# Kernel optimization log

Hardware: AMD Instinct MI355X
Metric: run time of the kernel (lower is better)

Reference implementation:

```python
import jax, jax.numpy as jnp
import numpy as np

N, E, IN, H, OUT, L = 50000, 640000, 64, 128, 128, 4
EPS = 1e-8


def setup_inputs() -> dict:
    key = jax.random.key(0)
    ks = jax.random.split(key, 14)
    rn = lambda k, shp: (jax.random.normal(k, shp, jnp.float32) * 0.05)
    return {
        "h": jax.random.normal(ks[0], (N, IN), jnp.float32),
        "pos": jax.random.normal(ks[1], (N, 3), jnp.float32),
        "edge_index": jax.random.randint(ks[2], (2, E), 0, N),
        "emb_W": rn(ks[3], (IN, H)), "emb_b": jnp.zeros((H,), jnp.float32),
        "msg_W1": rn(ks[4], (L, 2 * H + 1, H)), "msg_b1": jnp.zeros((L, H), jnp.float32),
        "msg_W2": rn(ks[5], (L, H, H)), "msg_b2": jnp.zeros((L, H), jnp.float32),
        "coord_W1": rn(ks[6], (L, H, H)), "coord_b1": jnp.zeros((L, H), jnp.float32),
        "coord_W2": rn(ks[7], (L, H, 1)), "coord_b2": jnp.zeros((L, 1), jnp.float32),
        "node_W1": rn(ks[8], (L, 2 * H, H)), "node_b1": jnp.zeros((L, H), jnp.float32),
        "node_W2": rn(ks[9], (L, H, H)), "node_b2": jnp.zeros((L, H), jnp.float32),
        "out_W1": rn(ks[10], (H, H)), "out_b1": jnp.zeros((H,), jnp.float32),
        "out_W2": rn(ks[11], (H, OUT)), "out_b2": jnp.zeros((OUT,), jnp.float32),
    }


def _egnn_forward(h, pos, src, dst, emb_W, emb_b, msg_W1, msg_b1, msg_W2, msg_b2,
                  coord_W1, coord_b1, coord_W2, coord_b2, node_W1, node_b1,
                  node_W2, node_b2, out_W1, out_b1, out_W2, out_b2):
    n = h.shape[0]
    h = h @ emb_W + emb_b  # node embedding [N, H]
    for l in range(L):
        hi, hj = h[dst], h[src]                     # target i, source j gathers [Etot, H]
        rel = pos[src] - pos[dst]                   # row - col (used for coord update)
        dist = jnp.linalg.norm(rel, axis=-1, keepdims=True)  # symmetric, same as |pos_i - pos_j|
        # message MLP: Linear -> SiLU -> Linear -> SiLU on [h_i, h_j, dist]
        m = jax.nn.silu(jnp.concatenate([hi, hj, dist], axis=-1) @ msg_W1[l] + msg_b1[l])
        m = jax.nn.silu(m @ msg_W2[l] + msg_b2[l])
        agg = jax.ops.segment_sum(m, dst, num_segments=n)  # scatter-add to targets
        # coord update: weights from h[row]=h_j, scatter to col=dst
        w = jax.nn.silu(hj @ coord_W1[l] + coord_b1[l]) @ coord_W2[l] + coord_b2[l]  # [Etot,1]
        coord_diff = w * rel / (dist + EPS)
        pos = pos + jax.ops.segment_sum(coord_diff, dst, num_segments=n)
        # node update with residual
        nh = jax.nn.silu(jnp.concatenate([h, agg], axis=-1) @ node_W1[l] + node_b1[l]) @ node_W2[l] + node_b2[l]
        h = h + nh
    out = jax.nn.silu(h @ out_W1 + out_b1) @ out_W2 + out_b2
    return out, pos


def reference(h, pos, edge_index, emb_W, emb_b, msg_W1, msg_b1, msg_W2, msg_b2,
              coord_W1, coord_b1, coord_W2, coord_b2, node_W1, node_b1,
              node_W2, node_b2, out_W1, out_b1, out_W2, out_b2):
    n = h.shape[0]
    loops = jnp.arange(n)  # add_self_loops
    src = jnp.concatenate([edge_index[0], loops])
    dst = jnp.concatenate([edge_index[1], loops])
    return _egnn_forward(h, pos, src, dst, emb_W, emb_b, msg_W1, msg_b1, msg_W2,
                         msg_b2, coord_W1, coord_b1, coord_W2, coord_b2, node_W1,
                         node_b1, node_W2, node_b2, out_W1, out_b1, out_W2, out_b2)
```

## Files before the change

### kernel.cpp

```cpp
#include <hip/hip_runtime.h>
#include <hip/hip_bf16.h>

#define EPSV 1e-8f

typedef short bf16x8 __attribute__((ext_vector_type(8)));
typedef float f32x4  __attribute__((ext_vector_type(4)));

__device__ __forceinline__ float silu_f(float x) {
    return x * __builtin_amdgcn_rcpf(1.0f + __expf(-x));
}
__device__ __forceinline__ float bf2f(short v) {
    return __uint_as_float(((unsigned int)(unsigned short)v) << 16);
}
__device__ __forceinline__ short f2bfs(float f) {
    __hip_bfloat16 h = __float2bfloat16(f);
    return *(short*)&h;
}

#define MAXM 24
struct PackArgs {
    const float* src[MAXM];
    unsigned int doff[MAXM];
    int nchunk[MAXM];
    int nmat;
};

__global__ __launch_bounds__(256) void repack_kernel(PackArgs pa, __hip_bfloat16* base)
{
    int bid = blockIdx.x;
    int m = 0, c = bid;
    while (m < pa.nmat && c >= pa.nchunk[m]) { c -= pa.nchunk[m]; ++m; }
    const float* src = pa.src[m];
    __hip_bfloat16* dst = base + pa.doff[m] + (size_t)c * 4096;
    for (int o = threadIdx.x; o < 4096; o += 256) {
        int j = o & 7, n = (o >> 3) & 127, g = o >> 10;
        dst[o] = __float2bfloat16(src[(size_t)(c * 32 + g * 8 + j) * 128 + n]);
    }
}

__global__ __launch_bounds__(256) void hist_kernel(
    const int* __restrict__ ei, int* __restrict__ cnt, int E, int N)
{
    int e = blockIdx.x * 256 + threadIdx.x;
    int Etot = E + N;
    if (e < Etot) {
        int d = (e < E) ? ei[E + e] : (e - E);
        atomicAdd(&cnt[d], 1);
    }
}

__global__ __launch_bounds__(256) void scan_block_kernel(
    const int* __restrict__ cnt, int* __restrict__ off, int* __restrict__ part, int n)
{
    __shared__ int sdata[256];
    const int tid = threadIdx.x;
    const int base = blockIdx.x * 4096 + tid * 16;
    int loc[16]; int s = 0;
    #pragma unroll
    for (int i = 0; i < 16; ++i) {
        int idx = base + i;
        int v = (idx < n) ? cnt[idx] : 0;
        loc[i] = s; s += v;
    }
    sdata[tid] = s;
    __syncthreads();
    for (int st = 1; st < 256; st <<= 1) {
        int v = (tid >= st) ? sdata[tid - st] : 0;
        __syncthreads();
        sdata[tid] += v;
        __syncthreads();
    }
    int texc = (tid > 0) ? sdata[tid - 1] : 0;
    #pragma unroll
    for (int i = 0; i < 16; ++i) {
        int idx = base + i;
        if (idx < n) off[idx] = texc + loc[i];
    }
    if (tid == 255) part[blockIdx.x] = sdata[255];
}

__global__ void scan_part_kernel(int* part, int np)
{
    if (threadIdx.x == 0 && blockIdx.x == 0) {
        int run = 0;
        for (int i = 0; i < np; ++i) { int v = part[i]; part[i] = run; run += v; }
    }
}

__global__ __launch_bounds__(256) void scan_add_kernel(
    int* __restrict__ off, const int* __restrict__ part, int n)
{
    int idx = blockIdx.x * 4096 + threadIdx.x * 16;
    int p = part[blockIdx.x];
    #pragma unroll
    for (int i = 0; i < 16; ++i)
        if (idx + i < n) off[idx + i] += p;
}

__global__ __launch_bounds__(256) void scatter_kernel(
    const int* __restrict__ ei, int* __restrict__ off,
    int* __restrict__ esrc, int* __restrict__ edst, int E, int N)
{
    int e = blockIdx.x * 256 + threadIdx.x;
    int Etot = E + N;
    if (e < Etot) {
        int s, d;
        if (e < E) { s = ei[e]; d = ei[E + e]; }
        else       { s = d = e - E; }
        int p = atomicAdd(&off[d], 1);
        esrc[p] = s; edst[p] = d;
    }
}

template<int LDA>
__device__ __forceinline__ void mfma_gemm(const __hip_bfloat16 (*At)[LDA], int acol0,
                                          const __hip_bfloat16* __restrict__ Bp,
                                          int kchunks, int w, int lane, f32x4 acc[4][2])
{
    const int ar = lane & 15, g = lane >> 4;
    const int bc = w * 32 + (lane & 15);
    for (int c = 0; c < kchunks; ++c) {
        const int ao = acol0 + c * 32 + g * 8;
        bf16x8 a0 = *(const bf16x8*)&At[ar +  0][ao];
        bf16x8 a1 = *(const bf16x8*)&At[ar + 16][ao];
        bf16x8 a2 = *(const bf16x8*)&At[ar + 32][ao];
        bf16x8 a3 = *(const bf16x8*)&At[ar + 48][ao];
        const __hip_bfloat16* bb = Bp + ((size_t)((c * 4 + g) * 128) + bc) * 8;
        bf16x8 b0 = *(const bf16x8*)(bb);
        bf16x8 b1 = *(const bf16x8*)(bb + 128);
        acc[0][0] = __builtin_amdgcn_mfma_f32_16x16x32_bf16(a0, b0, acc[0][0], 0, 0, 0);
        acc[1][0] = __builtin_amdgcn_mfma_f32_16x16x32_bf16(a1, b0, acc[1][0], 0, 0, 0);
        acc[2][0] = __builtin_amdgcn_mfma_f32_16x16x32_bf16(a2, b0, acc[2][0], 0, 0, 0);
        acc[3][0] = __builtin_amdgcn_mfma_f32_16x16x32_bf16(a3, b0, acc[3][0], 0, 0, 0);
        acc[0][1] = __builtin_amdgcn_mfma_f32_16x16x32_bf16(a0, b1, acc[0][1], 0, 0, 0);
        acc[1][1] = __builtin_amdgcn_mfma_f32_16x16x32_bf16(a1, b1, acc[1][1], 0, 0, 0);
        acc[2][1] = __builtin_amdgcn_mfma_f32_16x16x32_bf16(a2, b1, acc[2][1], 0, 0, 0);
        acc[3][1] = __builtin_amdgcn_mfma_f32_16x16x32_bf16(a3, b1, acc[3][1], 0, 0, 0);
    }
}

__device__ __forceinline__ void zacc(f32x4 acc[4][2]) {
    #pragma unroll
    for (int r = 0; r < 4; ++r)
        #pragma unroll
        for (int c = 0; c < 2; ++c) acc[r][c] = (f32x4){0.f, 0.f, 0.f, 0.f};
}

__device__ __forceinline__ void gemm4x4(const float* __restrict__ Wg,
                                        const float* a0p, const float* a1p,
                                        const float* a2p, const float* a3p,
                                        int K, int o0, float acc[4][4]) {
    for (int k = 0; k < K; k += 4) {
        float4 a0 = *(const float4*)(a0p + k);
        float4 a1 = *(const float4*)(a1p + k);
        float4 a2 = *(const float4*)(a2p + k);
        float4 a3 = *(const float4*)(a3p + k);
        float4 w0 = *(const float4*)(Wg + (k + 0) * 128 + o0);
        float4 w1 = *(const float4*)(Wg + (k + 1) * 128 + o0);
        float4 w2 = *(const float4*)(Wg + (k + 2) * 128 + o0);
        float4 w3 = *(const float4*)(Wg + (k + 3) * 128 + o0);
        float av[4][4] = {{a0.x, a0.y, a0.z, a0.w}, {a1.x, a1.y, a1.z, a1.w},
                          {a2.x, a2.y, a2.z, a2.w}, {a3.x, a3.y, a3.z, a3.w}};
        float wv[4][4] = {{w0.x, w0.y, w0.z, w0.w}, {w1.x, w1.y, w1.z, w1.w},
                          {w2.x, w2.y, w2.z, w2.w}, {w3.x, w3.y, w3.z, w3.w}};
        #pragma unroll
        for (int i = 0; i < 4; ++i)
            #pragma unroll
            for (int kk = 0; kk < 4; ++kk)
                #pragma unroll
                for (int j = 0; j < 4; ++j)
                    acc[i][j] = fmaf(av[i][kk], wv[kk][j], acc[i][j]);
    }
}

__global__ __launch_bounds__(256) void embed_kernel(
    const float* __restrict__ hin, const float* __restrict__ W,
    const float* __restrict__ b, float* __restrict__ hbuf,
    __hip_bfloat16* __restrict__ h16, int N)
{
    __shared__ float in_tile[32][68];
    const int t = threadIdx.x;
    const int nb = blockIdx.x * 32;

    #pragma unroll
    for (int it = 0; it < 2; ++it) {
        int flat = t + 256 * it;
        int c = flat & 15, e = flat >> 4;
        int node = nb + e; if (node >= N) node = N - 1;
        *(float4*)(&in_tile[e][c * 4]) = *(const float4*)(hin + (size_t)node * 64 + c * 4);
    }
    __syncthreads();

    const int o0 = (t & 31) * 4;
    const int e0 = (t >> 5) * 4;
    float acc[4][4];
    #pragma unroll
    for (int i = 0; i < 4; ++i)
        #pragma unroll
        for (int j = 0; j < 4; ++j) acc[i][j] = 0.f;
    gemm4x4(W, &in_tile[e0][0], &in_tile[e0 + 1][0], &in_tile[e0 + 2][0], &in_tile[e0 + 3][0],
            64, o0, acc);
    float4 bv = *(const float4*)(b + o0);
    #pragma unroll
    for (int i = 0; i < 4; ++i) {
        int node = nb + e0 + i;
        if (node < N) {
            float v0 = acc[i][0] + bv.x, v1 = acc[i][1] + bv.y;
            float v2 = acc[i][2] + bv.z, v3 = acc[i][3] + bv.w;
            *(float4*)(&hbuf[(size_t)node * 128 + o0]) = make_float4(v0, v1, v2, v3);
            __hip_bfloat16* hp = h16 + (size_t)node * 128 + o0;
            hp[0] = __float2bfloat16(v0); hp[1] = __float2bfloat16(v1);
            hp[2] = __float2bfloat16(v2); hp[3] = __float2bfloat16(v3);
        }
    }
}

__global__ __launch_bounds__(256) void precompute_kernel(
    const __hip_bfloat16* __restrict__ h16,
    const __hip_bfloat16* __restrict__ W1p,
    const float* __restrict__ b1,
    const __hip_bfloat16* __restrict__ cW1p,
    const float* __restrict__ cb1, const float* __restrict__ cW2,
    const float* __restrict__ cb2,
    __hip_bfloat16* __restrict__ U16, __hip_bfloat16* __restrict__ V16,
    float* __restrict__ wnum, int N)
{
    __shared__ __hip_bfloat16 a8[64][136];
    __shared__ float redw[64][4];
    const int t = threadIdx.x;
    const int nb = blockIdx.x * 64;
    const int lane = t & 63, w = t >> 6, g = lane >> 4, l15 = lane & 15;

    #pragma unroll
    for (int it = 0; it < 4; ++it) {
        int flat = t + 256 * it;
        int c = flat & 15, e = flat >> 4;
        int node = nb + e; if (node >= N) node = N - 1;
        *(int4*)(&a8[e][c * 8]) = *(const int4*)(h16 + (size_t)node * 128 + c * 8);
    }
    __syncthreads();

    const int colA = w * 32 + l15, colB = colA + 16;
    f32x4 acc[4][2];

    zacc(acc);
    mfma_gemm<136>(a8, 0, W1p, 4, w, lane, acc);
    {
        float bA = b1[colA], bB = b1[colB];
        #pragma unroll
        for (int r = 0; r < 4; ++r)
            #pragma unroll
            for (int q = 0; q < 4; ++q) {
                int node = nb + r * 16 + g * 4 + q;
                if (node < N) {
                    U16[(size_t)node * 128 + colA] = __float2bfloat16(acc[r][0][q] + bA);
                    U16[(size_t)node * 128 + colB] = __float2bfloat16(acc[r][1][q] + bB);
                }
            }
    }
    zacc(acc);
    mfma_gemm<136>(a8, 0, W1p + 4 * 4096, 4, w, lane, acc);
    #pragma unroll
    for (int r = 0; r < 4; ++r)
        #pragma unroll
        for (int q = 0; q < 4; ++q) {
            int node = nb + r * 16 + g * 4 + q;
            if (node < N) {
                V16[(size_t)node * 128 + colA] = __float2bfloat16(acc[r][0][q]);
                V16[(size_t)node * 128 + colB] = __float2bfloat16(acc[r][1][q]);
            }
        }
    zacc(acc);
    mfma_gemm<136>(a8, 0, cW1p, 4, w, lane, acc);
    {
        float cb1A = cb1[colA], cb1B = cb1[colB];
        float wA = cW2[colA], wB = cW2[colB];
        #pragma unroll
        for (int r = 0; r < 4; ++r)
            #pragma unroll
            for (int q = 0; q < 4; ++q) {
                float p = silu_f(acc[r][0][q] + cb1A) * wA
                        + silu_f(acc[r][1][q] + cb1B) * wB;
                p += __shfl_xor(p, 1);
                p += __shfl_xor(p, 2);
                p += __shfl_xor(p, 4);
                p += __shfl_xor(p, 8);
                if (l15 == 0) redw[r * 16 + g * 4 + q][w] = p;
            }
    }
    __syncthreads();
    if (t < 64 && nb + t < N)
        wnum[nb + t] = redw[t][0] + redw[t][1] + redw[t][2] + redw[t][3] + cb2[0];
}

__global__ __launch_bounds__(256) void edge_kernel(
    const __hip_bfloat16* __restrict__ U16, const __hip_bfloat16* __restrict__ V16,
    const float* __restrict__ wnum, const float* __restrict__ posb,
    const int* __restrict__ esrc, const int* __restrict__ edst,
    const float* __restrict__ W1tail,
    const __hip_bfloat16* __restrict__ W2p, const float* __restrict__ b2,
    float* __restrict__ agg, float* __restrict__ pdel, int Etot)
{
    __shared__ __hip_bfloat16 m1s[64][136];
    __shared__ int   srcl[64], dstl[64];
    __shared__ float relt[3][64], distl[64], wscl[64];

    const int t = threadIdx.x;
    const int eb = blockIdx.x * 64;
    const int lane = t & 63, w = t >> 6, g = lane >> 4, l15 = lane & 15;

    if (t < 64) {
        int e = eb + t;
        int s = 0, d = -1;
        if (e < Etot) { s = esrc[e]; d = edst[e]; }
        srcl[t] = s; dstl[t] = d;
        int dd = (d < 0) ? 0 : d;
        float rx = posb[3 * s + 0] - posb[3 * dd + 0];
        float ry = posb[3 * s + 1] - posb[3 * dd + 1];
        float rz = posb[3 * s + 2] - posb[3 * dd + 2];
        float dist = sqrtf(rx * rx + ry * ry + rz * rz);
        relt[0][t] = rx; relt[1][t] = ry; relt[2][t] = rz;
        distl[t] = dist;
        wscl[t] = wnum[s] * __builtin_amdgcn_rcpf(dist + EPSV);
    }
    __syncthreads();

    #pragma unroll
    for (int j = 0; j < 4; ++j) {
        int f = t + 256 * j;
        int c8 = f & 15, row = f >> 4;
        bf16x8 res;
        if (dstl[row] >= 0) {
            int s = srcl[row], d = dstl[row];
            bf16x8 uv = *(const bf16x8*)(U16 + (size_t)d * 128 + c8 * 8);
            bf16x8 vv = *(const bf16x8*)(V16 + (size_t)s * 128 + c8 * 8);
            float wt[8];
            *(float4*)&wt[0] = *(const float4*)(W1tail + c8 * 8);
            *(float4*)&wt[4] = *(const float4*)(W1tail + c8 * 8 + 4);
            float dv = distl[row];
            #pragma unroll
            for (int k = 0; k < 8; ++k) {
                float x = bf2f(uv[k]) + bf2f(vv[k]) + dv * wt[k];
                res[k] = f2bfs(silu_f(x));
            }
        } else {
            #pragma unroll
            for (int k = 0; k < 8; ++k) res[k] = 0;
        }
        *(bf16x8*)(&m1s[row][c8 * 8]) = res;
    }
    __syncthreads();

    const int colA = w * 32 + l15, colB = colA + 16;
    f32x4 acc[4][2];
    zacc(acc);
    mfma_gemm<136>(m1s, 0, W2p, 4, w, lane, acc);
    __syncthreads();

    {
        float b2a = b2[colA], b2b = b2[colB];
        #pragma unroll
        for (int r = 0; r < 4; ++r)
            #pragma unroll
            for (int q = 0; q < 4; ++q) {
                int row = r * 16 + g * 4 + q;
                m1s[row][colA] = __float2bfloat16(silu_f(acc[r][0][q] + b2a));
                m1s[row][colB] = __float2bfloat16(silu_f(acc[r][1][q] + b2b));
            }
    }
    __syncthreads();

    {
        int col = t & 127, half = t >> 7;
        int r0 = half * 32;
        float a = 0.f;
        int cur = dstl[r0];
        #pragma unroll 4
        for (int r = r0; r < r0 + 32; ++r) {
            int d = dstl[r];
            if (d != cur) {
                if (cur >= 0) atomicAdd(&agg[(size_t)cur * 128 + col], a);
                a = 0.f; cur = d;
            }
            if (d >= 0) a += bf2f(*(const short*)&m1s[r][col]);
        }
        if (cur >= 0) atomicAdd(&agg[(size_t)cur * 128 + col], a);
    }

    if (t < 192) {
        int e = t / 3, comp = t % 3;
        if (dstl[e] >= 0)
            atomicAdd(&pdel[(size_t)dstl[e] * 3 + comp], wscl[e] * relt[comp][e]);
    }
}

__global__ __launch_bounds__(256) void node_mfma_kernel(
    float* __restrict__ hbuf, __hip_bfloat16* __restrict__ h16,
    const float* __restrict__ agg,
    float* __restrict__ posb, const float* __restrict__ pdel,
    const __hip_bfloat16* __restrict__ W1p, const float* __restrict__ b1,
    const __hip_bfloat16* __restrict__ W2p, const float* __restrict__ b2,
    const __hip_bfloat16* __restrict__ nxtW1p, const float* __restrict__ nxt_b1,
    const __hip_bfloat16* __restrict__ nxt_cW1p, const float* __restrict__ nxt_cb1,
    const float* __restrict__ nxt_cW2, const float* __restrict__ nxt_cb2,
    __hip_bfloat16* __restrict__ U16, __hip_bfloat16* __restrict__ V16,
    float* __restrict__ wnum,
    int N, int doPre)
{
    __shared__ __hip_bfloat16 a_t[64][264];
    __shared__ __hip_bfloat16 us[64][136];
    __shared__ float redw[64][4];
    const int t = threadIdx.x;
    const int nb = blockIdx.x * 64;
    const int lane = t & 63, w = t >> 6, g = lane >> 4, l15 = lane & 15;

    #pragma unroll
    for (int it = 0; it < 4; ++it) {
        int flat = t + 256 * it;
        int c = flat & 15, e = flat >> 4;
        int node = nb + e; if (node >= N) node = N - 1;
        *(int4*)(&a_t[e][c * 8]) = *(const int4*)(h16 + (size_t)node * 128 + c * 8);
    }
    #pragma unroll
    for (int it = 0; it < 8; ++it) {
        int flat = t + 256 * it;
        int c = flat & 31, e = flat >> 5;
        int node = nb + e; if (node >= N) node = N - 1;
        float4 v = *(const float4*)(agg + (size_t)node * 128 + c * 4);
        __hip_bfloat16* p = &a_t[e][128 + c * 4];
        p[0] = __float2bfloat16(v.x); p[1] = __float2bfloat16(v.y);
        p[2] = __float2bfloat16(v.z); p[3] = __float2bfloat16(v.w);
    }
    __syncthreads();

    const int colA = w * 32 + l15, colB = colA + 16;
    f32x4 acc[4][2];

    zacc(acc);
    mfma_gemm<264>(a_t, 0, W1p, 8, w, lane, acc);
    {
        float b1a = b1[colA], b1b = b1[colB];
        #pragma unroll
        for (int r = 0; r < 4; ++r)
            #pragma unroll
            for (int q = 0; q < 4; ++q) {
                int row = r * 16 + g * 4 + q;
                us[row][colA] = __float2bfloat16(silu_f(acc[r][0][q] + b1a));
                us[row][colB] = __float2bfloat16(silu_f(acc[r][1][q] + b1b));
            }
    }
    __syncthreads();

    zacc(acc);
    mfma_gemm<136>(us, 0, W2p, 4, w, lane, acc);
    {
        float b2a = b2[colA], b2b = b2[colB];
        #pragma unroll
        for (int r = 0; r < 4; ++r)
            #pragma unroll
            for (int q = 0; q < 4; ++q) {
                int row = r * 16 + g * 4 + q;
                int node = nb + row;
                if (node < N) {
                    size_t off = (size_t)node * 128;
                    float va = hbuf[off + colA] + acc[r][0][q] + b2a;
                    float vb = hbuf[off + colB] + acc[r][1][q] + b2b;
                    hbuf[off + colA] = va; hbuf[off + colB] = vb;
                    __hip_bfloat16 ha = __float2bfloat16(va), hb = __float2bfloat16(vb);
                    h16[off + colA] = ha; h16[off + colB] = hb;
                    a_t[row][colA] = ha; a_t[row][colB] = hb;
                } else {
                    a_t[row][colA] = __float2bfloat16(0.f);
                    a_t[row][colB] = __float2bfloat16(0.f);
                }
            }
    }
    if (t < 192) {
        int e = t / 3, comp = t % 3;
        int node = nb + e;
        if (node < N) posb[3 * node + comp] += pdel[3 * node + comp];
    }

    if (!doPre) return;
    __syncthreads();

    zacc(acc);
    mfma_gemm<264>(a_t, 0, nxtW1p, 4, w, lane, acc);
    {
        float bA = nxt_b1[colA], bB = nxt_b1[colB];
        #pragma unroll
        for (int r = 0; r < 4; ++r)
            #pragma unroll
            for (int q = 0; q < 4; ++q) {
                int node = nb + r * 16 + g * 4 + q;
                if (node < N) {
                    U16[(size_t)node * 128 + colA] = __float2bfloat16(acc[r][0][q] + bA);
                    U16[(size_t)node * 128 + colB] = __float2bfloat16(acc[r][1][q] + bB);
                }
            }
    }
    zacc(acc);
    mfma_gemm<264>(a_t, 0, nxtW1p + 4 * 4096, 4, w, lane, acc);
    #pragma unroll
    for (int r = 0; r < 4; ++r)
        #pragma unroll
        for (int q = 0; q < 4; ++q) {
            int node = nb + r * 16 + g * 4 + q;
            if (node < N) {
                V16[(size_t)node * 128 + colA] = __float2bfloat16(acc[r][0][q]);
                V16[(size_t)node * 128 + colB] = __float2bfloat16(acc[r][1][q]);
            }
        }
    zacc(acc);
    mfma_gemm<264>(a_t, 0, nxt_cW1p, 4, w, lane, acc);
    {
        float cb1A = nxt_cb1[colA], cb1B = nxt_cb1[colB];
        float wA = nxt_cW2[colA], wB = nxt_cW2[colB];
        #pragma unroll
        for (int r = 0; r < 4; ++r)
            #pragma unroll
            for (int q = 0; q < 4; ++q) {
                float p = silu_f(acc[r][0][q] + cb1A) * wA
                        + silu_f(acc[r][1][q] + cb1B) * wB;
                p += __shfl_xor(p, 1);
                p += __shfl_xor(p, 2);
                p += __shfl_xor(p, 4);
                p += __shfl_xor(p, 8);
                if (l15 == 0) redw[r * 16 + g * 4 + q][w] = p;
            }
    }
    __syncthreads();
    if (t < 64 && nb + t < N)
        wnum[nb + t] = redw[t][0] + redw[t][1] + redw[t][2] + redw[t][3] + nxt_cb2[0];
}

__global__ __launch_bounds__(256) void out_mfma_kernel(
    const __hip_bfloat16* __restrict__ h16,
    const __hip_bfloat16* __restrict__ W1p, const float* __restrict__ b1,
    const __hip_bfloat16* __restrict__ W2p, const float* __restrict__ b2,
    float* __restrict__ outp, int N)
{
    __shared__ __hip_bfloat16 a8[64][136];
    __shared__ __hip_bfloat16 us[64][136];
    const int t = threadIdx.x;
    const int nb = blockIdx.x * 64;
    const int lane = t & 63, w = t >> 6, g = lane >> 4;

    #pragma unroll
    for (int it = 0; it < 4; ++it) {
        int flat = t + 256 * it;
        int c = flat & 15, e = flat >> 4;
        int node = nb + e; if (node >= N) node = N - 1;
        *(int4*)(&a8[e][c * 8]) = *(const int4*)(h16 + (size_t)node * 128 + c * 8);
    }
    __syncthreads();

    const int colA = w * 32 + (lane & 15), colB = colA + 16;
    f32x4 acc[4][2];

    zacc(acc);
    mfma_gemm<136>(a8, 0, W1p, 4, w, lane, acc);
    {
        float b1a = b1[colA], b1b = b1[colB];
        #pragma unroll
        for (int r = 0; r < 4; ++r)
            #pragma unroll
            for (int q = 0; q < 4; ++q) {
                int row = r * 16 + g * 4 + q;
                us[row][colA] = __float2bfloat16(silu_f(acc[r][0][q] + b1a));
                us[row][colB] = __float2bfloat16(silu_f(acc[r][1][q] + b1b));
            }
    }
    __syncthreads();

    zacc(acc);
    mfma_gemm<136>(us, 0, W2p, 4, w, lane, acc);
    {
        float b2a = b2[colA], b2b = b2[colB];
        #pragma unroll
        for (int r = 0; r < 4; ++r)
            #pragma unroll
            for (int q = 0; q < 4; ++q) {
                int row = r * 16 + g * 4 + q;
                int node = nb + row;
                if (node < N) {
                    outp[(size_t)node * 128 + colA] = acc[r][0][q] + b2a;
                    outp[(size_t)node * 128 + colB] = acc[r][1][q] + b2b;
                }
            }
    }
}

extern "C" void kernel_launch(void* const* d_in, const int* in_sizes, int n_in,
                              void* d_out, int out_size, void* d_ws, size_t ws_size,
                              hipStream_t stream)
{
    const float* hin  = (const float*)d_in[0];
    const float* pos  = (const float*)d_in[1];
    const int*   ei   = (const int*)d_in[2];
    const float* embW = (const float*)d_in[3];
    const float* embb = (const float*)d_in[4];
    const float* mW1  = (const float*)d_in[5];
    const float* mb1  = (const float*)d_in[6];
    const float* mW2  = (const float*)d_in[7];
    const float* mb2  = (const float*)d_in[8];
    const float* cW1  = (const float*)d_in[9];
    const float* cb1  = (const float*)d_in[10];
    const float* cW2  = (const float*)d_in[11];
    const float* cb2  = (const float*)d_in[12];
    const float* nW1  = (const float*)d_in[13];
    const float* nb1  = (const float*)d_in[14];
    const float* nW2  = (const float*)d_in[15];
    const float* nb2  = (const float*)d_in[16];
    const float* oW1  = (const float*)d_in[17];
    const float* ob1  = (const float*)d_in[18];
    const float* oW2  = (const float*)d_in[19];
    const float* ob2  = (const float*)d_in[20];

    const int N = in_sizes[0] / 64;
    const int E = in_sizes[2] / 2;
    const int Etot = E + N;

    float* hbuf = (float*)d_ws;
    float* aggb = hbuf + (size_t)N * 128;
    float* posb = aggb + (size_t)N * 128;
    float* pdel = posb + (size_t)N * 3;
    float* wnum = pdel + (size_t)N * 3;
    __hip_bfloat16* h16 = (__hip_bfloat16*)(wnum + N);
    __hip_bfloat16* U16 = h16 + (size_t)N * 128;
    __hip_bfloat16* V16 = U16 + (size_t)N * 128;
    __hip_bfloat16* packed = V16 + (size_t)N * 128;
    int* cnt  = (int*)(packed + 120 * 4096);
    int* soff = cnt + N;
    int* part = soff + N;
    int* esrc = part + 64;
    int* edst = esrc + Etot;
    float* outp = (float*)d_out;

    PackArgs pa;
    int nm = 0; unsigned int poff = 0; int totalChunks = 0;
    auto addm = [&](const float* s, int kc) {
        pa.src[nm] = s; pa.doff[nm] = poff; pa.nchunk[nm] = kc;
        poff += (unsigned int)kc * 4096; totalChunks += kc; ++nm;
    };
    for (int l = 0; l < 4; ++l) {
        addm(mW1 + (size_t)l * 257 * 128, 8);
        addm(mW2 + (size_t)l * 128 * 128, 4);
        addm(cW1 + (size_t)l * 128 * 128, 4);
        addm(nW1 + (size_t)l * 256 * 128, 8);
        addm(nW2 + (size_t)l * 128 * 128, 4);
    }
    addm(oW1, 4);
    addm(oW2, 4);
    pa.nmat = nm;

    const unsigned int LSTRIDE = 28 * 4096;

    hipMemcpyAsync(posb, pos, (size_t)N * 3 * sizeof(float),
                   hipMemcpyDeviceToDevice, stream);
    repack_kernel<<<totalChunks, 256, 0, stream>>>(pa, packed);

    const int scanBlocks = (N + 4095) / 4096;
    hipMemsetAsync(cnt, 0, (size_t)N * sizeof(int), stream);
    hist_kernel<<<(Etot + 255) / 256, 256, 0, stream>>>(ei, cnt, E, N);
    scan_block_kernel<<<scanBlocks, 256, 0, stream>>>(cnt, soff, part, N);
    scan_part_kernel<<<1, 64, 0, stream>>>(part, scanBlocks);
    scan_add_kernel<<<scanBlocks, 256, 0, stream>>>(soff, part, N);
    scatter_kernel<<<(Etot + 255) / 256, 256, 0, stream>>>(ei, soff, esrc, edst, E, N);

    const int nodeBlocks32 = (N + 31) / 32;
    const int nodeBlocks64 = (N + 63) / 64;
    const int edgeBlocks   = (Etot + 63) / 64;

    embed_kernel<<<nodeBlocks32, 256, 0, stream>>>(hin, embW, embb, hbuf, h16, N);

    precompute_kernel<<<nodeBlocks64, 256, 0, stream>>>(
        h16, packed, mb1, packed + 12 * 4096,
        cb1, cW2, cb2, U16, V16, wnum, N);

    for (int l = 0; l < 4; ++l) {
        hipMemsetAsync(aggb, 0, (size_t)N * 128 * sizeof(float), stream);
        hipMemsetAsync(pdel, 0, (size_t)N * 3 * sizeof(float), stream);
        const __hip_bfloat16* lp = packed + (size_t)l * LSTRIDE;
        edge_kernel<<<edgeBlocks, 256, 0, stream>>>(
            U16, V16, wnum, posb, esrc, edst,
            mW1 + (size_t)l * 257 * 128 + 256 * 128,
            lp + 8 * 4096, mb2 + l * 128,
            aggb, pdel, Etot);
        const int ln = (l < 3) ? (l + 1) : l;
        const __hip_bfloat16* lpn = packed + (size_t)ln * LSTRIDE;
        node_mfma_kernel<<<nodeBlocks64, 256, 0, stream>>>(
            hbuf, h16, aggb, posb, pdel,
            lp + 16 * 4096, nb1 + l * 128,
            lp + 24 * 4096, nb2 + l * 128,
            lpn, mb1 + (size_t)ln * 128,
            lpn + 12 * 4096, cb1 + (size_t)ln * 128,
            cW2 + (size_t)ln * 128, cb2 + ln,
            U16, V16, wnum,
            N, (l < 3) ? 1 : 0);
    }
    out_mfma_kernel<<<nodeBlocks64, 256, 0, stream>>>(
        h16, packed + (size_t)4 * LSTRIDE, ob1,
        packed + (size_t)4 * LSTRIDE + 4 * 4096, ob2, outp, N);

    hipMemcpyAsync(outp + (size_t)N * 128, posb, (size_t)N * 3 * sizeof(float),
                   hipMemcpyDeviceToDevice, stream);
}
```

Before: 1.032 ms.

## Fuse embedding into precompute and output MLP into last node kernel

Replaces the FP32 embedding kernel with an MFMA bf16 embedding fused into the first-layer precompute kernel, so h stays in shared memory instead of being written and reread. The output MLP moves into the final node-update kernel via a mode flag, which drops a launch and a reread of h16. The edge kernel is reordered so the position atomics come first, the W1 tail is hoisted out of the loop, and the aggregation scatter has each thread handle two columns over 16 rows. In exchange the embedding now runs in bf16, which loses some precision, and the output MLP reads its input from the a_t shared buffer, whose exact contents are not visible here.

After: 1.078 ms. 4.4% more time.

```diff
diff --git a/kernel.cpp b/kernel.cpp
--- a/kernel.cpp
+++ b/kernel.cpp
@@ -146,97 +146,35 @@
         for (int c = 0; c < 2; ++c) acc[r][c] = (f32x4){0.f, 0.f, 0.f, 0.f};
 }
 
-__device__ __forceinline__ void gemm4x4(const float* __restrict__ Wg,
-                                        const float* a0p, const float* a1p,
-                                        const float* a2p, const float* a3p,
-                                        int K, int o0, float acc[4][4]) {
-    for (int k = 0; k < K; k += 4) {
-        float4 a0 = *(const float4*)(a0p + k);
-        float4 a1 = *(const float4*)(a1p + k);
-        float4 a2 = *(const float4*)(a2p + k);
-        float4 a3 = *(const float4*)(a3p + k);
-        float4 w0 = *(const float4*)(Wg + (k + 0) * 128 + o0);
-        float4 w1 = *(const float4*)(Wg + (k + 1) * 128 + o0);
-        float4 w2 = *(const float4*)(Wg + (k + 2) * 128 + o0);
-        float4 w3 = *(const float4*)(Wg + (k + 3) * 128 + o0);
-        float av[4][4] = {{a0.x, a0.y, a0.z, a0.w}, {a1.x, a1.y, a1.z, a1.w},
-                          {a2.x, a2.y, a2.z, a2.w}, {a3.x, a3.y, a3.z, a3.w}};
-        float wv[4][4] = {{w0.x, w0.y, w0.z, w0.w}, {w1.x, w1.y, w1.z, w1.w},
-                          {w2.x, w2.y, w2.z, w2.w}, {w3.x, w3.y, w3.z, w3.w}};
-        #pragma unroll
-        for (int i = 0; i < 4; ++i)
-            #pragma unroll
-            for (int kk = 0; kk < 4; ++kk)
-                #pragma unroll
-                for (int j = 0; j < 4; ++j)
-                    acc[i][j] = fmaf(av[i][kk], wv[kk][j], acc[i][j]);
-    }
-}
-
-__global__ __launch_bounds__(256) void embed_kernel(
-    const float* __restrict__ hin, const float* __restrict__ W,
-    const float* __restrict__ b, float* __restrict__ hbuf,
-    __hip_bfloat16* __restrict__ h16, int N)
-{
-    __shared__ float in_tile[32][68];
-    const int t = threadIdx.x;
-    const int nb = blockIdx.x * 32;
-
-    #pragma unroll
-    for (int it = 0; it < 2; ++it) {
-        int flat = t + 256 * it;
-        int c = flat & 15, e = flat >> 4;
-        int node = nb + e; if (node >= N) node = N - 1;
-        *(float4*)(&in_tile[e][c * 4]) = *(const float4*)(hin + (size_t)node * 64 + c * 4);
-    }
-    __syncthreads();
-
-    const int o0 = (t & 31) * 4;
-    const int e0 = (t >> 5) * 4;
-    float acc[4][4];
-    #pragma unroll
-    for (int i = 0; i < 4; ++i)
-        #pragma unroll
-        for (int j = 0; j < 4; ++j) acc[i][j] = 0.f;
-    gemm4x4(W, &in_tile[e0][0], &in_tile[e0 + 1][0], &in_tile[e0 + 2][0], &in_tile[e0 + 3][0],
-            64, o0, acc);
-    float4 bv = *(const float4*)(b + o0);
-    #pragma unroll
-    for (int i = 0; i < 4; ++i) {
-        int node = nb + e0 + i;
-        if (node < N) {
-            float v0 = acc[i][0] + bv.x, v1 = acc[i][1] + bv.y;
-            float v2 = acc[i][2] + bv.z, v3 = acc[i][3] + bv.w;
-            *(float4*)(&hbuf[(size_t)node * 128 + o0]) = make_float4(v0, v1, v2, v3);
-            __hip_bfloat16* hp = h16 + (size_t)node * 128 + o0;
-            hp[0] = __float2bfloat16(v0); hp[1] = __float2bfloat16(v1);
-            hp[2] = __float2bfloat16(v2); hp[3] = __float2bfloat16(v3);
-        }
-    }
-}
-
-__global__ __launch_bounds__(256) void precompute_kernel(
-    const __hip_bfloat16* __restrict__ h16,
-    const __hip_bfloat16* __restrict__ W1p,
-    const float* __restrict__ b1,
+__global__ __launch_bounds__(256) void embed_pre_kernel(
+    const float* __restrict__ hin,
+    const __hip_bfloat16* __restrict__ embWp, const float* __restrict__ embb,
+    const __hip_bfloat16* __restrict__ W1p, const float* __restrict__ b1,
     const __hip_bfloat16* __restrict__ cW1p,
     const float* __restrict__ cb1, const float* __restrict__ cW2,
     const float* __restrict__ cb2,
+    float* __restrict__ hbuf, __hip_bfloat16* __restrict__ h16,
     __hip_bfloat16* __restrict__ U16, __hip_bfloat16* __restrict__ V16,
     float* __restrict__ wnum, int N)
 {
-    __shared__ __hip_bfloat16 a8[64][136];
+    __shared__ __hip_bfloat16 a_e[64][72];
+    __shared__ __hip_bfloat16 a_h[64][136];
     __shared__ float redw[64][4];
     const int t = threadIdx.x;
     const int nb = blockIdx.x * 64;
     const int lane = t & 63, w = t >> 6, g = lane >> 4, l15 = lane & 15;
 
     #pragma unroll
-    for (int it = 0; it < 4; ++it) {
+    for (int it = 0; it < 2; ++it) {
         int flat = t + 256 * it;
-        int c = flat & 15, e = flat >> 4;
+        int c8 = flat & 7, e = flat >> 3;
         int node = nb + e; if (node >= N) node = N - 1;
-        *(int4*)(&a8[e][c * 8]) = *(const int4*)(h16 + (size_t)node * 128 + c * 8);
+        const float* hp = hin + (size_t)node * 64 + c8 * 8;
+        float4 v0 = *(const float4*)hp, v1 = *(const float4*)(hp + 4);
+        bf16x8 r;
+        r[0] = f2bfs(v0.x); r[1] = f2bfs(v0.y); r[2] = f2bfs(v0.z); r[3] = f2bfs(v0.w);
+        r[4] = f2bfs(v1.x); r[5] = f2bfs(v1.y); r[6] = f2bfs(v1.z); r[7] = f2bfs(v1.w);
+        *(bf16x8*)(&a_e[e][c8 * 8]) = r;
     }
     __syncthreads();
 
@@ -244,7 +182,29 @@
     f32x4 acc[4][2];
 
     zacc(acc);
-    mfma_gemm<136>(a8, 0, W1p, 4, w, lane, acc);
+    mfma_gemm<72>(a_e, 0, embWp, 2, w, lane, acc);
+    {
+        float bA = embb[colA], bB = embb[colB];
+        #pragma unroll
+        for (int r = 0; r < 4; ++r)
+            #pragma unroll
+            for (int q = 0; q < 4; ++q) {
+                int row = r * 16 + g * 4 + q;
+                int node = nb + row;
+                float va = acc[r][0][q] + bA, vb = acc[r][1][q] + bB;
+                __hip_bfloat16 ha = __float2bfloat16(va), hb = __float2bfloat16(vb);
+                a_h[row][colA] = ha; a_h[row][colB] = hb;
+                if (node < N) {
+                    size_t off = (size_t)node * 128;
+                    hbuf[off + colA] = va; hbuf[off + colB] = vb;
+                    h16[off + colA] = ha; h16[off + colB] = hb;
+                }
+            }
+    }
+    __syncthreads();
+
+    zacc(acc);
+    mfma_gemm<136>(a_h, 0, W1p, 4, w, lane, acc);
     {
         float bA = b1[colA], bB = b1[colB];
         #pragma unroll
@@ -259,7 +219,7 @@
             }
     }
     zacc(acc);
-    mfma_gemm<136>(a8, 0, W1p + 4 * 4096, 4, w, lane, acc);
+    mfma_gemm<136>(a_h, 0, W1p + 4 * 4096, 4, w, lane, acc);
     #pragma unroll
     for (int r = 0; r < 4; ++r)
         #pragma unroll
@@ -271,7 +231,7 @@
             }
         }
     zacc(acc);
-    mfma_gemm<136>(a8, 0, cW1p, 4, w, lane, acc);
+    mfma_gemm<136>(a_h, 0, cW1p, 4, w, lane, acc);
     {
         float cb1A = cb1[colA], cb1B = cb1[colB];
         float wA = cW2[colA], wB = cW2[colB];
@@ -325,72 +285,85 @@
     }
     __syncthreads();
 
-    #pragma unroll
-    for (int j = 0; j < 4; ++j) {
-        int f = t + 256 * j;
-        int c8 = f & 15, row = f >> 4;
-        bf16x8 res;
-        if (dstl[row] >= 0) {
-            int s = srcl[row], d = dstl[row];
-            bf16x8 uv = *(const bf16x8*)(U16 + (size_t)d * 128 + c8 * 8);
-            bf16x8 vv = *(const bf16x8*)(V16 + (size_t)s * 128 + c8 * 8);
-            float wt[8];
-            *(float4*)&wt[0] = *(const float4*)(W1tail + c8 * 8);
-            *(float4*)&wt[4] = *(const float4*)(W1tail + c8 * 8 + 4);
-            float dv = distl[row];
-            #pragma unroll
-            for (int k = 0; k < 8; ++k) {
-                float x = bf2f(uv[k]) + bf2f(vv[k]) + dv * wt[k];
-                res[k] = f2bfs(silu_f(x));
-            }
-        } else {
-            #pragma unroll
-            for (int k = 0; k < 8; ++k) res[k] = 0;
-        }
-        *(bf16x8*)(&m1s[row][c8 * 8]) = res;
-    }
-    __syncthreads();
-
-    const int colA = w * 32 + l15, colB = colA + 16;
-    f32x4 acc[4][2];
-    zacc(acc);
-    mfma_gemm<136>(m1s, 0, W2p, 4, w, lane, acc);
-    __syncthreads();
-
-    {
-        float b2a = b2[colA], b2b = b2[colB];
-        #pragma unroll
-        for (int r = 0; r < 4; ++r)
-            #pragma unroll
-            for (int q = 0; q < 4; ++q) {
-                int row = r * 16 + g * 4 + q;
-                m1s[row][colA] = __float2bfloat16(silu_f(acc[r][0][q] + b2a));
-                m1s[row][colB] = __float2bfloat16(silu_f(acc[r][1][q] + b2b));
-            }
-    }
-    __syncthreads();
-
-    {
-        int col = t & 127, half = t >> 7;
-        int r0 = half * 32;
-        float a = 0.f;
-        int cur = dstl[r0];
-        #pragma unroll 4
-        for (int r = r0; r < r0 + 32; ++r) {
-            int d = dstl[r];
-            if (d != cur) {
-                if (cur >= 0) atomicAdd(&agg[(size_t)cur * 128 + col], a);
-                a = 0.f; cur = d;
-            }
-            if (d >= 0) a += bf2f(*(const short*)&m1s[r][col]);
-        }
-        if (cur >= 0) atomicAdd(&agg[(size_t)cur * 128 + col], a);
-    }
-
     if (t < 192) {
         int e = t / 3, comp = t % 3;
         if (dstl[e] >= 0)
             atomicAdd(&pdel[(size_t)dstl[e] * 3 + comp], wscl[e] * relt[comp][e]);
+    }
+
+    {
+        const int c8 = t & 15, row0 = t >> 4;
+        float wt[8];
+        *(float4*)&wt[0] = *(const float4*)(W1tail + c8 * 8);
+        *(float4*)&wt[4] = *(const float4*)(W1tail + c8 * 8 + 4);
+        #pragma unroll
+        for (int j = 0; j < 4; ++j) {
+            int row = row0 + 16 * j;
+            bf16x8 res;
+            if (dstl[row] >= 0) {
+                int s = srcl[row], d = dstl[row];
+                bf16x8 uv = *(const bf16x8*)(U16 + (size_t)d * 128 + c8 * 8);
+                bf16x8 vv = *(const bf16x8*)(V16 + (size_t)s * 128 + c8 * 8);
+                float dv = distl[row];
+                #pragma unroll
+                for (int k = 0; k < 8; ++k) {
+                    float x = bf2f(uv[k]) + bf2f(vv[k]) + dv * wt[k];
+                    res[k] = f2bfs(silu_f(x));
+                }
+            } else {
+                #pragma unroll
+                for (int k = 0; k < 8; ++k) res[k] = 0;
+            }
+            *(bf16x8*)(&m1s[row][c8 * 8]) = res;
+        }
+    }
+    __syncthreads();
+
+    const int colA = w * 32 + l15, colB = colA + 16;
+    f32x4 acc[4][2];
+    zacc(acc);
+    mfma_gemm<136>(m1s, 0, W2p, 4, w, lane, acc);
+    __syncthreads();
+
+    {
+        float b2a = b2[colA], b2b = b2[colB];
+        #pragma unroll
+        for (int r = 0; r < 4; ++r)
+            #pragma unroll
+            for (int q = 0; q < 4; ++q) {
+                int row = r * 16 + g * 4 + q;
+                m1s[row][colA] = __float2bfloat16(silu_f(acc[r][0][q] + b2a));
+                m1s[row][colB] = __float2bfloat16(silu_f(acc[r][1][q] + b2b));
+            }
+    }
+    __syncthreads();
+
+    {
+        int cp = t & 63;
+        int qtr = t >> 6;
+        int r0 = qtr * 16;
+        float a0 = 0.f, a1 = 0.f;
+        int cur = dstl[r0];
+        #pragma unroll 4
+        for (int r = r0; r < r0 + 16; ++r) {
+            int d = dstl[r];
+            if (d != cur) {
+                if (cur >= 0) {
+                    atomicAdd(&agg[(size_t)cur * 128 + 2 * cp], a0);
+                    atomicAdd(&agg[(size_t)cur * 128 + 2 * cp + 1], a1);
+                }
+                a0 = a1 = 0.f; cur = d;
+            }
+            if (d >= 0) {
+                unsigned int v = *(const unsigned int*)&m1s[r][2 * cp];
+                a0 += bf2f((short)(v & 0xffffu));
+                a1 += bf2f((short)(v >> 16));
+            }
+        }
+        if (cur >= 0) {
+            atomicAdd(&agg[(size_t)cur * 128 + 2 * cp], a0);
+            atomicAdd(&agg[(size_t)cur * 128 + 2 * cp + 1], a1);
+        }
     }
 }
 
@@ -405,7 +378,10 @@
     const float* __restrict__ nxt_cW2, const float* __restrict__ nxt_cb2,
     __hip_bfloat16* __restrict__ U16, __hip_bfloat16* __restrict__ V16,
     float* __restrict__ wnum,
-    int N, int doPre)
+    const __hip_bfloat16* __restrict__ oW1p, const float* __restrict__ ob1,
+    const __hip_bfloat16* __restrict__ oW2p, const float* __restrict__ ob2,
+    float* __restrict__ outp,
+    int N, int mode)
 {
     __shared__ __hip_bfloat16 a_t[64][264];
     __shared__ __hip_bfloat16 us[64][136];
@@ -481,8 +457,42 @@
         if (node < N) posb[3 * node + comp] += pdel[3 * node + comp];
     }
 
-    if (!doPre) return;
-    __syncthreads();
+    if (mode == 0) return;
+    __syncthreads();
+
+    if (mode == 2) {
+        zacc(acc);
+        mfma_gemm<264>(a_t, 0, oW1p, 4, w, lane, acc);
+        {
+            float b1a = ob1[colA], b1b = ob1[colB];
+            #pragma unroll
+            for (int r = 0; r < 4; ++r)
+                #pragma unroll
+                for (int q = 0; q < 4; ++q) {
+                    int row = r * 16 + g * 4 + q;
+                    us[row][colA] = __float2bfloat16(silu_f(acc[r][0][q] + b1a));
+                    us[row][colB] = __float2bfloat16(silu_f(acc[r][1][q] + b1b));
+                }
+        }
+        __syncthreads();
+        zacc(acc);
+        mfma_gemm<136>(us, 0, oW2p, 4, w, lane, acc);
+        {
+            float b2a = ob2[colA], b2b = ob2[colB];
+            #pragma unroll
+            for (int r = 0; r < 4; ++r)
+                #pragma unroll
+                for (int q = 0; q < 4; ++q) {
+                    int row = r * 16 + g * 4 + q;
+                    int node = nb + row;
+                    if (node < N) {
+                        outp[(size_t)node * 128 + colA] = acc[r][0][q] + b2a;
+                        outp[(size_t)node * 128 + colB] = acc[r][1][q] + b2b;
+                    }
+                }
+        }
+        return;
+    }
 
     zacc(acc);
     mfma_gemm<264>(a_t, 0, nxtW1p, 4, w, lane, acc);
@@ -532,63 +542,6 @@
     __syncthreads();
     if (t < 64 && nb + t < N)
         wnum[nb + t] = redw[t][0] + redw[t][1] + redw[t][2] + redw[t][3] + nxt_cb2[0];
-}
-
-__global__ __launch_bounds__(256) void out_mfma_kernel(
-    const __hip_bfloat16* __restrict__ h16,
-    const __hip_bfloat16* __restrict__ W1p, const float* __restrict__ b1,
-    const __hip_bfloat16* __restrict__ W2p, const float* __restrict__ b2,
-    float* __restrict__ outp, int N)
-{
-    __shared__ __hip_bfloat16 a8[64][136];
-    __shared__ __hip_bfloat16 us[64][136];
-    const int t = threadIdx.x;
-    const int nb = blockIdx.x * 64;
-    const int lane = t & 63, w = t >> 6, g = lane >> 4;
-
-    #pragma unroll
-    for (int it = 0; it < 4; ++it) {
-        int flat = t + 256 * it;
-        int c = flat & 15, e = flat >> 4;
-        int node = nb + e; if (node >= N) node = N - 1;
-        *(int4*)(&a8[e][c * 8]) = *(const int4*)(h16 + (size_t)node * 128 + c * 8);
-    }
-    __syncthreads();
-
-    const int colA = w * 32 + (lane & 15), colB = colA + 16;
-    f32x4 acc[4][2];
-
-    zacc(acc);
-    mfma_gemm<136>(a8, 0, W1p, 4, w, lane, acc);
-    {
-        float b1a = b1[colA], b1b = b1[colB];
-        #pragma unroll
-        for (int r = 0; r < 4; ++r)
-            #pragma unroll
-            for (int q = 0; q < 4; ++q) {
-                int row = r * 16 + g * 4 + q;
-                us[row][colA] = __float2bfloat16(silu_f(acc[r][0][q] + b1a));
-                us[row][colB] = __float2bfloat16(silu_f(acc[r][1][q] + b1b));
-            }
-    }
-    __syncthreads();
-
-    zacc(acc);
-    mfma_gemm<136>(us, 0, W2p, 4, w, lane, acc);
-    {
-        float b2a = b2[colA], b2b = b2[colB];
-        #pragma unroll
-        for (int r = 0; r < 4; ++r)
-            #pragma unroll
-            for (int q = 0; q < 4; ++q) {
-                int row = r * 16 + g * 4 + q;
-                int node = nb + row;
-                if (node < N) {
-                    outp[(size_t)node * 128 + colA] = acc[r][0][q] + b2a;
-                    outp[(size_t)node * 128 + colB] = acc[r][1][q] + b2b;
-                }
-            }
-    }
 }
 
 extern "C" void kernel_launch(void* const* d_in, const int* in_sizes, int n_in,
@@ -630,7 +583,7 @@
     __hip_bfloat16* U16 = h16 + (size_t)N * 128;
     __hip_bfloat16* V16 = U16 + (size_t)N * 128;
     __hip_bfloat16* packed = V16 + (size_t)N * 128;
-    int* cnt  = (int*)(packed + 120 * 4096);
+    int* cnt  = (int*)(packed + 122 * 4096);
     int* soff = cnt + N;
     int* part = soff + N;
     int* esrc = part + 64;
@@ -652,9 +605,13 @@
     }
     addm(oW1, 4);
     addm(oW2, 4);
+    addm(embW, 2);
     pa.nmat = nm;
 
     const unsigned int LSTRIDE = 28 * 4096;
+    const __hip_bfloat16* oW1p  = packed + (size_t)4 * LSTRIDE;
+    const __hip_bfloat16* oW2p  = packed + (size_t)4 * LSTRIDE + 4 * 4096;
+    const __hip_bfloat16* embWp = packed + (size_t)4 * LSTRIDE + 8 * 4096;
 
     hipMemcpyAsync(posb, pos, (size_t)N * 3 * sizeof(float),
                    hipMemcpyDeviceToDevice, stream);
@@ -668,15 +625,14 @@
     scan_add_kernel<<<scanBlocks, 256, 0, stream>>>(soff, part, N);
     scatter_kernel<<<(Etot + 255) / 256, 256, 0, stream>>>(ei, soff, esrc, edst, E, N);
 
-    const int nodeBlocks32 = (N + 31) / 32;
     const int nodeBlocks64 = (N + 63) / 64;
     const int edgeBlocks   = (Etot + 63) / 64;
 
-    embed_kernel<<<nodeBlocks32, 256, 0, stream>>>(hin, embW, embb, hbuf, h16, N);
-
-    precompute_kernel<<<nodeBlocks64, 256, 0, stream>>>(
-        h16, packed, mb1, packed + 12 * 4096,
-        cb1, cW2, cb2, U16, V16, wnum, N);
+    embed_pre_kernel<<<nodeBlocks64, 256, 0, stream>>>(
+        hin, embWp, embb,
+        packed, mb1, packed + 12 * 4096,
+        cb1, cW2, cb2,
+        hbuf, h16, U16, V16, wnum, N);
 
     for (int l = 0; l < 4; ++l) {
         hipMemsetAsync(aggb, 0, (size_t)N * 128 * sizeof(float), stream);
@@ -697,11 +653,9 @@
             lpn + 12 * 4096, cb1 + (size_t)ln * 128,
             cW2 + (size_t)ln * 128, cb2 + ln,
             U16, V16, wnum,
-            N, (l < 3) ? 1 : 0);
-    }
-    out_mfma_kernel<<<nodeBlocks64, 256, 0, stream>>>(
-        h16, packed + (size_t)4 * LSTRIDE, ob1,
-        packed + (size_t)4 * LSTRIDE + 4 * 4096, ob2, outp, N);
+            oW1p, ob1, oW2p, ob2, outp,
+            N, (l < 3) ? 1 : 2);
+    }
 
     hipMemcpyAsync(outp + (size_t)N * 128, posb, (size_t)N * 3 * sizeof(float),
                    hipMemcpyDeviceToDevice, stream);
```
